# Optimization experiments

Measured on AMD Instinct MI355X. Metric: run time of the kernel, lower is better.

The kernel has to match this reference:

```python
import jax, jax.numpy as jnp
import numpy as np

N = 200000
E = 5000000


def _gcn_norm(edge_index, num_nodes):
    # add self-loops and compute symmetric normalization (PyG GCNConv default)
    loop = jnp.arange(num_nodes, dtype=edge_index.dtype)
    src = jnp.concatenate([edge_index[0], loop])
    dst = jnp.concatenate([edge_index[1], loop])
    ones = jnp.ones(dst.shape[0], dtype=jnp.float32)
    deg = jax.ops.segment_sum(ones, dst, num_segments=num_nodes)
    dis = jnp.where(deg > 0, jax.lax.rsqrt(deg), 0.0)
    norm = dis[src] * dis[dst]  # [E+N]
    return src, dst, norm


def _gcn_layer(x, src, dst, norm, W, b, num_nodes):
    xl = x @ W  # [N, out] dense linear (no bias, PyG default)
    msg = xl[src] * norm[:, None]  # gather + scale
    agg = jax.ops.segment_sum(msg, dst, num_segments=num_nodes)  # scatter-add
    return agg + b


def setup_inputs() -> dict:
    key = jax.random.key(0)
    ks = jax.random.split(key, 10)
    x = jax.random.normal(ks[0], (N, 12), dtype=jnp.float32)
    edge_index = jax.random.randint(ks[1], (2, E), 0, N, dtype=jnp.int64)
    def glorot(k, fi, fo):
        s = np.sqrt(6.0 / (fi + fo)).astype(np.float32)
        return jax.random.uniform(k, (fi, fo), jnp.float32, -s, s)
    return {
        "x": x,
        "edge_index": edge_index,
        "W1": glorot(ks[2], 12, 16), "b1": jnp.zeros((16,), jnp.float32),
        "W2": glorot(ks[3], 16, 8), "b2": jnp.zeros((8,), jnp.float32),
        "W3": glorot(ks[4], 8, 16), "b3": jnp.zeros((16,), jnp.float32),
        "W4": glorot(ks[5], 16, 12), "b4": jnp.zeros((12,), jnp.float32),
    }


def reference(x, edge_index, W1, b1, W2, b2, W3, b3, W4, b4):
    num_nodes = x.shape[0]
    src, dst, norm = _gcn_norm(edge_index, num_nodes)
    # Encoder
    h = jax.nn.relu(_gcn_layer(x, src, dst, norm, W1, b1, num_nodes))
    h = _gcn_layer(h, src, dst, norm, W2, b2, num_nodes)
    # Decoder
    h = jax.nn.relu(_gcn_layer(h, src, dst, norm, W3, b3, num_nodes))
    h = jax.nn.sigmoid(_gcn_layer(h, src, dst, norm, W4, b4, num_nodes))
    return h
```

## Files before the change

### kernel.cpp

```cpp
#include <hip/hip_runtime.h>
#include <hip/hip_fp16.h>
#include <math.h>


#define NPB 1024
#define MAX_NB 256
#define CAP 26496
#define BIN_CHUNK 4096
#define BIN_TH 512
#define EPT (BIN_CHUNK / BIN_TH)
#define MAXB CAP

__global__ void init_cur_kernel(int* __restrict__ bucket_cur, int NB) {
    int t = blockIdx.x * blockDim.x + threadIdx.x;
    if (t < NB) bucket_cur[t] = t * CAP;
}

__global__ __launch_bounds__(BIN_TH) void bin_kernel(const int* __restrict__ src,
                                                     const int* __restrict__ dst,
                                                     int* __restrict__ bucket_cur,
                                                     unsigned int* __restrict__ binned,
                                                     int E, int NB) {
    __shared__ int h[MAX_NB];
    __shared__ int scl[MAX_NB + 1];
    __shared__ int base[MAX_NB];
    __shared__ int sscan[256];
    __shared__ unsigned int stage[BIN_CHUNK];
    __shared__ unsigned char bkt8[BIN_CHUNK];
    int cbeg = blockIdx.x * BIN_CHUNK;
    int cend = min(cbeg + BIN_CHUNK, E);
    int chunk_n = cend - cbeg;
    int tid = threadIdx.x;

    for (int t = tid; t < NB; t += BIN_TH) h[t] = 0;
    __syncthreads();
    int myd[EPT];
#pragma unroll
    for (int j = 0; j < EPT; j++) {
        int e = cbeg + tid + j * BIN_TH;
        if (e < cend) {
            myd[j] = dst[e];
            atomicAdd(&h[myd[j] >> 10], 1);
        }
    }
    __syncthreads();
    int v = (tid < NB) ? h[tid] : 0;
    if (tid < 256) sscan[tid] = v;
    __syncthreads();
    for (int off = 1; off < 256; off <<= 1) {
        int t = (tid >= off && tid < 256) ? sscan[tid - off] : 0;
        __syncthreads();
        if (tid < 256) sscan[tid] += t;
        __syncthreads();
    }
    if (tid < NB) {
        scl[tid] = sscan[tid] - v;
        base[tid] = v ? atomicAdd(&bucket_cur[tid], v) : 0;
    }
    if (tid == 0) scl[NB] = chunk_n;
    __syncthreads();
    for (int t = tid; t < NB; t += BIN_TH) h[t] = 0;
    __syncthreads();
#pragma unroll
    for (int j = 0; j < EPT; j++) {
        int e = cbeg + tid + j * BIN_TH;
        if (e < cend) {
            int d = myd[j];
            int bkt = d >> 10;
            int pos = scl[bkt] + atomicAdd(&h[bkt], 1);
            stage[pos] = ((unsigned)src[e] << 10) | (unsigned)(d & 1023);
            bkt8[pos] = (unsigned char)bkt;
        }
    }
    __syncthreads();
    for (int k = tid; k < chunk_n; k += BIN_TH) {
        int bkt = bkt8[k];
        binned[base[bkt] + (k - scl[bkt])] = stage[k];
    }
}

__global__ __launch_bounds__(1024) void csr_bucket_t1_kernel(
    const unsigned int* __restrict__ binned,
    const int* __restrict__ bucket_cur,
    int2* __restrict__ rows, int* __restrict__ mids, float* __restrict__ dis,
    int* __restrict__ col,
    const float* __restrict__ x,
    __half* __restrict__ xls, int N, int halfN) {
    __shared__ int cnt[NPB];
    __shared__ int cnt0[NPB];
    __shared__ int curA[NPB];
    __shared__ int curB[NPB];
    __shared__ int colbuf[MAXB];
    int b = blockIdx.x;
    int nbase = b << 10;
    int nlocal = min(NPB, N - nbase);
    int beg = b * CAP;
    int bsize = bucket_cur[b] - beg;
    int tid = threadIdx.x;

    cnt[tid] = 0;
    cnt0[tid] = 0;
    __syncthreads();
    for (int k = tid; k < bsize; k += 1024) {
        unsigned rec = binned[beg + k];
        int l = rec & 1023u;
        int s = (int)(rec >> 10);
        atomicAdd(&cnt[l], 1);
        if (s < halfN) atomicAdd(&cnt0[l], 1);
    }
    __syncthreads();
    int v = cnt[tid];
    int v0 = cnt0[tid];
    curA[tid] = v;
    __syncthreads();
    for (int off = 1; off < 1024; off <<= 1) {
        int t = (tid >= off) ? curA[tid - off] : 0;
        __syncthreads();
        curA[tid] += t;
        __syncthreads();
    }
    int excl = curA[tid] - v;
    float d = 1.0f / sqrtf((float)(v + 1));
    if (tid < nlocal) {
        rows[nbase + tid] = make_int2(beg + excl, beg + excl + v);
        mids[nbase + tid] = beg + excl + v0;
        dis[nbase + tid] = d;
    }
    __syncthreads();
    curA[tid] = excl;
    curB[tid] = excl + v0;
    __syncthreads();
    if (bsize <= MAXB) {
        for (int k = tid; k < bsize; k += 1024) {
            unsigned rec = binned[beg + k];
            int l = rec & 1023u;
            int s = (int)(rec >> 10);
            int pos = (s < halfN) ? atomicAdd(&curA[l], 1)
                                  : atomicAdd(&curB[l], 1);
            colbuf[pos] = s;
        }
        __syncthreads();
        for (int k = tid; k < bsize; k += 1024) col[beg + k] = colbuf[k];
    } else {
        for (int k = tid; k < bsize; k += 1024) {
            unsigned rec = binned[beg + k];
            int l = rec & 1023u;
            int s = (int)(rec >> 10);
            int pos = (s < halfN) ? atomicAdd(&curA[l], 1)
                                  : atomicAdd(&curB[l], 1);
            col[beg + pos] = s;
        }
    }
    if (tid < nlocal) {
        int i = nbase + tid;
        float h[12];
#pragma unroll
        for (int k = 0; k < 12; k++) h[k] = x[(size_t)i * 12 + k];
        __half2* x2 = (__half2*)xls;
#pragma unroll
        for (int k = 0; k < 6; k++) {
            x2[(size_t)i * 8 + k] =
                __floats2half2_rn(h[2 * k] * d, h[2 * k + 1] * d);
        }
    }
}

template <int P, int S>
__device__ __forceinline__ void acc_node(const __half2* __restrict__ x2, int c,
                                         float2 (&acc)[P]) {
    __half2 t[P];
#pragma unroll
    for (int k = 0; k < P; k++) t[k] = x2[(size_t)c * S + k];
#pragma unroll
    for (int k = 0; k < P; k++) {
        float2 v = __half22float2(t[k]);
        acc[k].x += v.x;
        acc[k].y += v.y;
    }
}

template <int P, int S>
__device__ __forceinline__ void acc_quad(const __half2* __restrict__ x2, int4 c,
                                         float2 (&acc)[P]) {
    __half2 t[4][P];
#pragma unroll
    for (int k = 0; k < P; k++) t[0][k] = x2[(size_t)c.x * S + k];
#pragma unroll
    for (int k = 0; k < P; k++) t[1][k] = x2[(size_t)c.y * S + k];
#pragma unroll
    for (int k = 0; k < P; k++) t[2][k] = x2[(size_t)c.z * S + k];
#pragma unroll
    for (int k = 0; k < P; k++) t[3][k] = x2[(size_t)c.w * S + k];
#pragma unroll
    for (int k = 0; k < P; k++) {
        float2 a0 = __half22float2(t[0][k]), a1 = __half22float2(t[1][k]);
        float2 a2 = __half22float2(t[2][k]), a3 = __half22float2(t[3][k]);
        acc[k].x += (a0.x + a1.x) + (a2.x + a3.x);
        acc[k].y += (a0.y + a1.y) + (a2.y + a3.y);
    }
}

template <int C, int S>
__device__ __forceinline__ void gather_acc_rng(
    int i, int p, int beg, int end, bool self,
    const int* __restrict__ col, const __half2* __restrict__ x2,
    float2 (&acc)[C / 2]) {
    constexpr int P = C / 2;
    constexpr int UN = (P >= 6) ? 2 : 3;
#pragma unroll
    for (int k = 0; k < P; k++) {
        if (self && p == 0) acc[k] = __half22float2(x2[(size_t)i * S + k]);
        else acc[k] = make_float2(0.0f, 0.0f);
    }
    int nedge = end - beg;
    int pre = (4 - (beg & 3)) & 3;
    if (pre > nedge) pre = nedge;
    for (int j = p; j < pre; j += 2) acc_node<P, S>(x2, col[beg + j], acc);
    int abeg = beg + pre;
    int nq = (end - abeg) >> 2;
    int q = p;
    for (; q + 2 * (UN - 1) < nq; q += 2 * UN) {
        int4 cs[UN];
#pragma unroll
        for (int u = 0; u < UN; u++)
            cs[u] = *reinterpret_cast<const int4*>(col + abeg + 4 * (q + 2 * u));
#pragma unroll
        for (int u = 0; u < UN; u++) acc_quad<P, S>(x2, cs[u], acc);
    }
    for (; q < nq; q += 2) {
        int4 ca = *reinterpret_cast<const int4*>(col + abeg + 4 * q);
        acc_quad<P, S>(x2, ca, acc);
    }
    int tbeg = abeg + 4 * nq;
    for (int j = tbeg + p; j < end; j += 2) acc_node<P, S>(x2, col[j], acc);
#pragma unroll
    for (int k = 0; k < P; k++) {
        acc[k].x += __shfl_xor(acc[k].x, 1);
        acc[k].y += __shfl_xor(acc[k].y, 1);
    }
}

__global__ __launch_bounds__(256) void gather12h_kernel(
    const int2* __restrict__ rows, const int* __restrict__ mids,
    const int* __restrict__ col, const __half* __restrict__ xin,
    float* __restrict__ part0, float* __restrict__ part1, int N, int halfN) {
    int grp = blockIdx.x >> 3;
    int sub = blockIdx.x & 7;
    int chunk = sub >> 2;
    int range = (grp << 2) + (sub & 3);
    int t2 = range * 256 + (int)threadIdx.x;
    int i = t2 >> 1;
    int p = t2 & 1;
    if (i >= N) return;
    int2 r = rows[i];
    int m = mids[i];
    int beg = chunk ? m : r.x;
    int end = chunk ? r.y : m;
    bool self = chunk ? (i >= halfN) : (i < halfN);
    float2 acc[6];
    gather_acc_rng<12, 8>(i, p, beg, end, self, col, (const __half2*)xin, acc);
    float* part = chunk ? part1 : part0;
    float2* ap = (float2*)(part + (size_t)i * 12);
#pragma unroll
    for (int k = 0; k < 6; k++) {
        if ((k & 1) == p) ap[k] = acc[k];
    }
}

__global__ __launch_bounds__(256) void transform12_kernel(
    const float* __restrict__ p0, const float* __restrict__ p1,
    const float* __restrict__ b1, const float* __restrict__ W1,
    const float* __restrict__ W2, const float* __restrict__ dis,
    __half* __restrict__ xout, int N) {
    __shared__ float sW1[12 * 16];
    __shared__ float sW2[16 * 8];
    __shared__ float sB[16];
    if (threadIdx.x < 192) sW1[threadIdx.x] = W1[threadIdx.x];
    if (threadIdx.x < 128) sW2[threadIdx.x] = W2[threadIdx.x];
    if (threadIdx.x < 16) sB[threadIdx.x] = b1[threadIdx.x];
    __syncthreads();
    int i = blockIdx.x * blockDim.x + threadIdx.x;
    if (i >= N) return;
    float d = dis[i];
    float A[12];
    const float4* a4 = (const float4*)(p0 + (size_t)i * 12);
    const float4* b4 = (const float4*)(p1 + (size_t)i * 12);
#pragma unroll
    for (int q = 0; q < 3; q++) {
        float4 va = a4[q], vb = b4[q];
        A[4 * q + 0] = (va.x + vb.x) * d;
        A[4 * q + 1] = (va.y + vb.y) * d;
        A[4 * q + 2] = (va.z + vb.z) * d;
        A[4 * q + 3] = (va.w + vb.w) * d;
    }
    float h[16];
#pragma unroll
    for (int f = 0; f < 16; f++) {
        float acc = sB[f];
#pragma unroll
        for (int k = 0; k < 12; k++) acc = fmaf(A[k], sW1[k * 16 + f], acc);
        h[f] = fmaxf(acc, 0.0f);
    }
    __half2* x2 = (__half2*)xout;
#pragma unroll
    for (int k2 = 0; k2 < 4; k2++) {
        float o0 = 0.0f, o1 = 0.0f;
#pragma unroll
        for (int k = 0; k < 16; k++) {
            o0 = fmaf(h[k], sW2[k * 8 + 2 * k2], o0);
            o1 = fmaf(h[k], sW2[k * 8 + 2 * k2 + 1], o1);
        }
        x2[(size_t)i * 4 + k2] = __floats2half2_rn(o0 * d, o1 * d);
    }
}

__global__ __launch_bounds__(256) void gather8_t3_kernel(
    const int2* __restrict__ rows, const int* __restrict__ col,
    const float* __restrict__ dis, const __half* __restrict__ xin,
    const float* __restrict__ b2, __half* __restrict__ xout, int N) {
    int tid = blockIdx.x * blockDim.x + threadIdx.x;
    int i = tid >> 1;
    int p = tid & 1;
    if (i >= N) return;
    int2 r = rows[i];
    float2 acc[4];
    gather_acc_rng<8, 4>(i, p, r.x, r.y, true, col, (const __half2*)xin, acc);
    float d = dis[i];
    __half2* x2o = (__half2*)xout;
#pragma unroll
    for (int k = 0; k < 4; k++) {
        if ((k >> 1) == p) {
            x2o[(size_t)i * 4 + k] =
                __floats2half2_rn((acc[k].x * d + b2[2 * k]) * d,
                                  (acc[k].y * d + b2[2 * k + 1]) * d);
        }
    }
}

__global__ __launch_bounds__(256) void gather8_t4_kernel(
    const int2* __restrict__ rows, const int* __restrict__ col,
    const float* __restrict__ dis, const __half* __restrict__ xin,
    const float* __restrict__ b3, const float* __restrict__ W3,
    const float* __restrict__ W4, __half* __restrict__ xout, int N) {
    __shared__ float sW3[8 * 16];
    __shared__ float sW4[16 * 12];
    __shared__ float sB[16];
    if (threadIdx.x < 128) sW3[threadIdx.x] = W3[threadIdx.x];
    if (threadIdx.x < 192) sW4[threadIdx.x] = W4[threadIdx.x];
    if (threadIdx.x < 16) sB[threadIdx.x] = b3[threadIdx.x];
    __syncthreads();
    int tid = blockIdx.x * blockDim.x + threadIdx.x;
    int i = tid >> 1;
    int p = tid & 1;
    if (i >= N) return;
    int2 r = rows[i];
    float2 acc[4];
    gather_acc_rng<8, 4>(i, p, r.x, r.y, true, col, (const __half2*)xin, acc);
    float d = dis[i];
    float A[8];
#pragma unroll
    for (int k = 0; k < 4; k++) {
        A[2 * k] = acc[k].x * d;
        A[2 * k + 1] = acc[k].y * d;
    }
    float h[8];
#pragma unroll
    for (int f = 0; f < 8; f++) {
        float a = sB[p * 8 + f];
#pragma unroll
        for (int k = 0; k < 8; k++) a = fmaf(A[k], sW3[k * 16 + p * 8 + f], a);
        h[f] = fmaxf(a, 0.0f);
    }
    float o[12];
#pragma unroll
    for (int j = 0; j < 12; j++) {
        float a = 0.0f;
#pragma unroll
        for (int f = 0; f < 8; f++) a = fmaf(h[f], sW4[(p * 8 + f) * 12 + j], a);
        o[j] = a;
    }
#pragma unroll
    for (int j = 0; j < 12; j++) o[j] += __shfl_xor(o[j], 1);
    __half2* x2o = (__half2*)xout;
    if (p == 0) {
#pragma unroll
        for (int k = 0; k < 4; k++) {
            x2o[(size_t)i * 8 + k] =
                __floats2half2_rn(o[2 * k] * d, o[2 * k + 1] * d);
        }
    } else {
#pragma unroll
        for (int k = 0; k < 2; k++) {
            x2o[(size_t)i * 8 + 4 + k] =
                __floats2half2_rn(o[8 + 2 * k] * d, o[9 + 2 * k] * d);
        }
    }
}

__global__ __launch_bounds__(256) void combine_sig_kernel(
    const float* __restrict__ p0, const float* __restrict__ p1,
    const float* __restrict__ dis, const float* __restrict__ bias,
    float* __restrict__ out, int N) {
    __shared__ float sB[12];
    if (threadIdx.x < 12) sB[threadIdx.x] = bias[threadIdx.x];
    __syncthreads();
    int i = blockIdx.x * blockDim.x + threadIdx.x;
    if (i >= N) return;
    float d = dis[i];
    const float4* a4 = (const float4*)(p0 + (size_t)i * 12);
    const float4* b4 = (const float4*)(p1 + (size_t)i * 12);
    float4* o4 = (float4*)(out + (size_t)i * 12);
#pragma unroll
    for (int q = 0; q < 3; q++) {
        float4 va = a4[q], vb = b4[q];
        float4 r;
        r.x = 1.0f / (1.0f + expf(-((va.x + vb.x) * d + sB[4 * q + 0])));
        r.y = 1.0f / (1.0f + expf(-((va.y + vb.y) * d + sB[4 * q + 1])));
        r.z = 1.0f / (1.0f + expf(-((va.z + vb.z) * d + sB[4 * q + 2])));
        r.w = 1.0f / (1.0f + expf(-((va.w + vb.w) * d + sB[4 * q + 3])));
        o4[q] = r;
    }
}

static inline size_t align_up(size_t v, size_t a) { return (v + a - 1) & ~(a - 1); }

extern "C" void kernel_launch(void* const* d_in, const int* in_sizes, int n_in,
                              void* d_out, int out_size, void* d_ws, size_t ws_size,
                              hipStream_t stream) {
    const float* x  = (const float*)d_in[0];
    const int*   ei = (const int*)d_in[1];
    const float* W1 = (const float*)d_in[2];
    const float* b1 = (const float*)d_in[3];
    const float* W2 = (const float*)d_in[4];
    const float* b2 = (const float*)d_in[5];
    const float* W3 = (const float*)d_in[6];
    const float* b3 = (const float*)d_in[7];
    const float* W4 = (const float*)d_in[8];
    const float* b4 = (const float*)d_in[9];
    float* out = (float*)d_out;

    const int N = in_sizes[0] / 12;
    const int E = in_sizes[1] / 2;
    const int halfN = N >> 1;
    const int* src = ei;
    const int* dst = ei + E;
    const int NB = (N + NPB - 1) / NPB;

    char* ws = (char*)d_ws;
    size_t off = 0;
    int* bucket_cur = (int*)(ws + off);   off = align_up(off + (size_t)NB * 4, 256);
    int2* rows = (int2*)(ws + off);       off = align_up(off + (size_t)N * 8, 256);
    int* mids = (int*)(ws + off);         off = align_up(off + (size_t)N * 4, 256);
    float* dis = (float*)(ws + off);      off = align_up(off + (size_t)N * 4, 256);
    unsigned int* binned = (unsigned int*)(ws + off);
    off = align_up(off + ((size_t)NB * CAP + 4096) * 4, 256);
    int* col = (int*)(ws + off);          off = align_up(off + ((size_t)NB * CAP + 4096) * 4, 256);
    __half* xls = (__half*)(ws + off);    off = align_up(off + (size_t)N * 16 * 2, 256);
    __half* xls2 = (__half*)(ws + off);   off = align_up(off + (size_t)N * 16 * 2, 256);
    (void)ws_size; (void)n_in; (void)out_size;

    float* part0 = (float*)binned;
    float* part1 = part0 + (size_t)N * 12;

    const int B = 256;
    auto blocks = [&](long long n) { return (int)((n + B - 1) / B); };
    int nb2 = blocks(2LL * N);
    nb2 = (nb2 + 3) & ~3;
    const int G2 = nb2 * 2;

    init_cur_kernel<<<1, 256, 0, stream>>>(bucket_cur, NB);
    bin_kernel<<<(E + BIN_CHUNK - 1) / BIN_CHUNK, BIN_TH, 0, stream>>>(src, dst, bucket_cur, binned, E, NB);
    csr_bucket_t1_kernel<<<NB, 1024, 0, stream>>>(binned, bucket_cur, rows, mids, dis,
                                                  col, x, xls, N, halfN);

    gather12h_kernel<<<G2, B, 0, stream>>>(rows, mids, col, xls, part0, part1, N, halfN);

    transform12_kernel<<<blocks(N), B, 0, stream>>>(part0, part1, b1, W1, W2, dis, xls2, N);

    gather8_t3_kernel<<<blocks(2LL * N), B, 0, stream>>>(rows, col, dis, xls2, b2, xls, N);

    gather8_t4_kernel<<<blocks(2LL * N), B, 0, stream>>>(rows, col, dis, xls, b3, W3, W4,
                                                         xls2, N);

    gather12h_kernel<<<G2, B, 0, stream>>>(rows, mids, col, xls2, part0, part1, N, halfN);

    combine_sig_kernel<<<blocks(N), B, 0, stream>>>(part0, part1, dis, b4, out, N);
}
```

Measured before the change: 360.4 us.

## Split 12-wide gathers into four source-range chunks for cache locality

The CSR build now sorts each row's neighbors into four source-node quarter ranges instead of halves and records the three split points per node. The 12-feature gather kernels can run one pass per quarter, so each pass touches a smaller slice of the fp16 feature table and should hit cache more often. Partial sums go to four buffers that the transform and sigmoid kernels add together. The costs are more blocks, extra partial-buffer traffic, an integer divide per edge, and a fallback to two chunks when the workspace is too small.

New measurement: 365.6 us. Within noise of the previous version (+1.4%).

```diff
diff --git a/kernel.cpp b/kernel.cpp
--- a/kernel.cpp
+++ b/kernel.cpp
@@ -82,14 +82,12 @@
 __global__ __launch_bounds__(1024) void csr_bucket_t1_kernel(
     const unsigned int* __restrict__ binned,
     const int* __restrict__ bucket_cur,
-    int2* __restrict__ rows, int* __restrict__ mids, float* __restrict__ dis,
+    int2* __restrict__ rows, int4* __restrict__ qmids, float* __restrict__ dis,
     int* __restrict__ col,
     const float* __restrict__ x,
-    __half* __restrict__ xls, int N, int halfN) {
-    __shared__ int cnt[NPB];
-    __shared__ int cnt0[NPB];
-    __shared__ int curA[NPB];
-    __shared__ int curB[NPB];
+    __half* __restrict__ xls, int N, int qN) {
+    __shared__ int cnt4[4 * NPB];
+    __shared__ int sc[NPB];
     __shared__ int colbuf[MAXB];
     int b = blockIdx.x;
     int nbase = b << 10;
@@ -98,45 +96,51 @@
     int bsize = bucket_cur[b] - beg;
     int tid = threadIdx.x;
 
-    cnt[tid] = 0;
-    cnt0[tid] = 0;
+    for (int t = tid; t < 4 * NPB; t += 1024) cnt4[t] = 0;
     __syncthreads();
     for (int k = tid; k < bsize; k += 1024) {
         unsigned rec = binned[beg + k];
         int l = rec & 1023u;
         int s = (int)(rec >> 10);
-        atomicAdd(&cnt[l], 1);
-        if (s < halfN) atomicAdd(&cnt0[l], 1);
-    }
-    __syncthreads();
-    int v = cnt[tid];
-    int v0 = cnt0[tid];
-    curA[tid] = v;
+        int q = s / qN;
+        atomicAdd(&cnt4[q * NPB + l], 1);
+    }
+    __syncthreads();
+    int c0 = cnt4[tid];
+    int c1 = cnt4[NPB + tid];
+    int c2 = cnt4[2 * NPB + tid];
+    int c3 = cnt4[3 * NPB + tid];
+    int v = c0 + c1 + c2 + c3;
+    sc[tid] = v;
     __syncthreads();
     for (int off = 1; off < 1024; off <<= 1) {
-        int t = (tid >= off) ? curA[tid - off] : 0;
+        int t = (tid >= off) ? sc[tid - off] : 0;
         __syncthreads();
-        curA[tid] += t;
+        sc[tid] += t;
         __syncthreads();
     }
-    int excl = curA[tid] - v;
+    int excl = sc[tid] - v;
     float d = 1.0f / sqrtf((float)(v + 1));
     if (tid < nlocal) {
         rows[nbase + tid] = make_int2(beg + excl, beg + excl + v);
-        mids[nbase + tid] = beg + excl + v0;
+        qmids[nbase + tid] = make_int4(beg + excl + c0,
+                                       beg + excl + c0 + c1,
+                                       beg + excl + c0 + c1 + c2, 0);
         dis[nbase + tid] = d;
     }
     __syncthreads();
-    curA[tid] = excl;
-    curB[tid] = excl + v0;
+    cnt4[tid] = excl;
+    cnt4[NPB + tid] = excl + c0;
+    cnt4[2 * NPB + tid] = excl + c0 + c1;
+    cnt4[3 * NPB + tid] = excl + c0 + c1 + c2;
     __syncthreads();
     if (bsize <= MAXB) {
         for (int k = tid; k < bsize; k += 1024) {
             unsigned rec = binned[beg + k];
             int l = rec & 1023u;
             int s = (int)(rec >> 10);
-            int pos = (s < halfN) ? atomicAdd(&curA[l], 1)
-                                  : atomicAdd(&curB[l], 1);
+            int q = s / qN;
+            int pos = atomicAdd(&cnt4[q * NPB + l], 1);
             colbuf[pos] = s;
         }
         __syncthreads();
@@ -146,8 +150,8 @@
             unsigned rec = binned[beg + k];
             int l = rec & 1023u;
             int s = (int)(rec >> 10);
-            int pos = (s < halfN) ? atomicAdd(&curA[l], 1)
-                                  : atomicAdd(&curB[l], 1);
+            int q = s / qN;
+            int pos = atomicAdd(&cnt4[q * NPB + l], 1);
             col[beg + pos] = s;
         }
     }
@@ -240,26 +244,42 @@
     }
 }
 
-__global__ __launch_bounds__(256) void gather12h_kernel(
-    const int2* __restrict__ rows, const int* __restrict__ mids,
+template <int NC>
+__global__ __launch_bounds__(256) void gather12p_kernel(
+    const int2* __restrict__ rows, const int4* __restrict__ qmids,
     const int* __restrict__ col, const __half* __restrict__ xin,
-    float* __restrict__ part0, float* __restrict__ part1, int N, int halfN) {
+    float* __restrict__ part0, float* __restrict__ part1,
+    float* __restrict__ part2, float* __restrict__ part3, int N, int qN) {
     int grp = blockIdx.x >> 3;
     int sub = blockIdx.x & 7;
-    int chunk = sub >> 2;
-    int range = (grp << 2) + (sub & 3);
+    int chunk, range;
+    if (NC == 4) {
+        chunk = sub >> 1;
+        range = (grp << 1) + (sub & 1);
+    } else {
+        chunk = sub >> 2;
+        range = (grp << 2) + (sub & 3);
+    }
     int t2 = range * 256 + (int)threadIdx.x;
     int i = t2 >> 1;
     int p = t2 & 1;
     if (i >= N) return;
     int2 r = rows[i];
-    int m = mids[i];
-    int beg = chunk ? m : r.x;
-    int end = chunk ? r.y : m;
-    bool self = chunk ? (i >= halfN) : (i < halfN);
+    int4 qm = qmids[i];
+    int beg, end;
+    if (NC == 4) {
+        beg = (chunk == 0) ? r.x : (chunk == 1) ? qm.x : (chunk == 2) ? qm.y : qm.z;
+        end = (chunk == 0) ? qm.x : (chunk == 1) ? qm.y : (chunk == 2) ? qm.z : r.y;
+    } else {
+        beg = chunk ? qm.y : r.x;
+        end = chunk ? r.y : qm.y;
+    }
+    int qi = i / qN;
+    bool self = (NC == 4) ? (qi == chunk) : ((qi >> 1) == chunk);
     float2 acc[6];
     gather_acc_rng<12, 8>(i, p, beg, end, self, col, (const __half2*)xin, acc);
-    float* part = chunk ? part1 : part0;
+    float* part = (chunk == 0) ? part0 : (chunk == 1) ? part1
+                 : (chunk == 2) ? part2 : part3;
     float2* ap = (float2*)(part + (size_t)i * 12);
 #pragma unroll
     for (int k = 0; k < 6; k++) {
@@ -267,8 +287,10 @@
     }
 }
 
+template <int NP>
 __global__ __launch_bounds__(256) void transform12_kernel(
     const float* __restrict__ p0, const float* __restrict__ p1,
+    const float* __restrict__ p2, const float* __restrict__ p3,
     const float* __restrict__ b1, const float* __restrict__ W1,
     const float* __restrict__ W2, const float* __restrict__ dis,
     __half* __restrict__ xout, int N) {
@@ -283,15 +305,21 @@
     if (i >= N) return;
     float d = dis[i];
     float A[12];
-    const float4* a4 = (const float4*)(p0 + (size_t)i * 12);
-    const float4* b4 = (const float4*)(p1 + (size_t)i * 12);
 #pragma unroll
     for (int q = 0; q < 3; q++) {
-        float4 va = a4[q], vb = b4[q];
-        A[4 * q + 0] = (va.x + vb.x) * d;
-        A[4 * q + 1] = (va.y + vb.y) * d;
-        A[4 * q + 2] = (va.z + vb.z) * d;
-        A[4 * q + 3] = (va.w + vb.w) * d;
+        float4 va = ((const float4*)(p0 + (size_t)i * 12))[q];
+        float4 vb = ((const float4*)(p1 + (size_t)i * 12))[q];
+        float sx = va.x + vb.x, sy = va.y + vb.y, sz = va.z + vb.z, sw = va.w + vb.w;
+        if (NP == 4) {
+            float4 vc = ((const float4*)(p2 + (size_t)i * 12))[q];
+            float4 vd = ((const float4*)(p3 + (size_t)i * 12))[q];
+            sx += vc.x + vd.x; sy += vc.y + vd.y;
+            sz += vc.z + vd.z; sw += vc.w + vd.w;
+        }
+        A[4 * q + 0] = sx * d;
+        A[4 * q + 1] = sy * d;
+        A[4 * q + 2] = sz * d;
+        A[4 * q + 3] = sw * d;
     }
     float h[16];
 #pragma unroll
@@ -397,8 +425,10 @@
     }
 }
 
+template <int NP>
 __global__ __launch_bounds__(256) void combine_sig_kernel(
     const float* __restrict__ p0, const float* __restrict__ p1,
+    const float* __restrict__ p2, const float* __restrict__ p3,
     const float* __restrict__ dis, const float* __restrict__ bias,
     float* __restrict__ out, int N) {
     __shared__ float sB[12];
@@ -407,17 +437,23 @@
     int i = blockIdx.x * blockDim.x + threadIdx.x;
     if (i >= N) return;
     float d = dis[i];
-    const float4* a4 = (const float4*)(p0 + (size_t)i * 12);
-    const float4* b4 = (const float4*)(p1 + (size_t)i * 12);
     float4* o4 = (float4*)(out + (size_t)i * 12);
 #pragma unroll
     for (int q = 0; q < 3; q++) {
-        float4 va = a4[q], vb = b4[q];
+        float4 va = ((const float4*)(p0 + (size_t)i * 12))[q];
+        float4 vb = ((const float4*)(p1 + (size_t)i * 12))[q];
+        float sx = va.x + vb.x, sy = va.y + vb.y, sz = va.z + vb.z, sw = va.w + vb.w;
+        if (NP == 4) {
+            float4 vc = ((const float4*)(p2 + (size_t)i * 12))[q];
+            float4 vd = ((const float4*)(p3 + (size_t)i * 12))[q];
+            sx += vc.x + vd.x; sy += vc.y + vd.y;
+            sz += vc.z + vd.z; sw += vc.w + vd.w;
+        }
         float4 r;
-        r.x = 1.0f / (1.0f + expf(-((va.x + vb.x) * d + sB[4 * q + 0])));
-        r.y = 1.0f / (1.0f + expf(-((va.y + vb.y) * d + sB[4 * q + 1])));
-        r.z = 1.0f / (1.0f + expf(-((va.z + vb.z) * d + sB[4 * q + 2])));
-        r.w = 1.0f / (1.0f + expf(-((va.w + vb.w) * d + sB[4 * q + 3])));
+        r.x = 1.0f / (1.0f + expf(-(sx * d + sB[4 * q + 0])));
+        r.y = 1.0f / (1.0f + expf(-(sy * d + sB[4 * q + 1])));
+        r.z = 1.0f / (1.0f + expf(-(sz * d + sB[4 * q + 2])));
+        r.w = 1.0f / (1.0f + expf(-(sw * d + sB[4 * q + 3])));
         o4[q] = r;
     }
 }
@@ -441,7 +477,7 @@
 
     const int N = in_sizes[0] / 12;
     const int E = in_sizes[1] / 2;
-    const int halfN = N >> 1;
+    const int qN = (N + 3) >> 2;
     const int* src = ei;
     const int* dst = ei + E;
     const int NB = (N + NPB - 1) / NPB;
@@ -450,39 +486,59 @@
     size_t off = 0;
     int* bucket_cur = (int*)(ws + off);   off = align_up(off + (size_t)NB * 4, 256);
     int2* rows = (int2*)(ws + off);       off = align_up(off + (size_t)N * 8, 256);
-    int* mids = (int*)(ws + off);         off = align_up(off + (size_t)N * 4, 256);
+    int4* qmids = (int4*)(ws + off);      off = align_up(off + (size_t)N * 16, 256);
     float* dis = (float*)(ws + off);      off = align_up(off + (size_t)N * 4, 256);
     unsigned int* binned = (unsigned int*)(ws + off);
     off = align_up(off + ((size_t)NB * CAP + 4096) * 4, 256);
     int* col = (int*)(ws + off);          off = align_up(off + ((size_t)NB * CAP + 4096) * 4, 256);
     __half* xls = (__half*)(ws + off);    off = align_up(off + (size_t)N * 16 * 2, 256);
     __half* xls2 = (__half*)(ws + off);   off = align_up(off + (size_t)N * 16 * 2, 256);
-    (void)ws_size; (void)n_in; (void)out_size;
+    size_t off23 = off;
+    float* part2 = (float*)(ws + off23);
+    size_t off_end = align_up(off23 + (size_t)N * 24 * 4, 256);
+    const bool use4 = (off_end <= ws_size);
+    float* part3 = part2 + (size_t)N * 12;
+    (void)n_in; (void)out_size;
 
     float* part0 = (float*)binned;
     float* part1 = part0 + (size_t)N * 12;
 
     const int B = 256;
     auto blocks = [&](long long n) { return (int)((n + B - 1) / B); };
-    int nb2 = blocks(2LL * N);
-    nb2 = (nb2 + 3) & ~3;
-    const int G2 = nb2 * 2;
+    int R = blocks(2LL * N);
+    R = (R + 3) & ~3;
 
     init_cur_kernel<<<1, 256, 0, stream>>>(bucket_cur, NB);
     bin_kernel<<<(E + BIN_CHUNK - 1) / BIN_CHUNK, BIN_TH, 0, stream>>>(src, dst, bucket_cur, binned, E, NB);
-    csr_bucket_t1_kernel<<<NB, 1024, 0, stream>>>(binned, bucket_cur, rows, mids, dis,
-                                                  col, x, xls, N, halfN);
-
-    gather12h_kernel<<<G2, B, 0, stream>>>(rows, mids, col, xls, part0, part1, N, halfN);
-
-    transform12_kernel<<<blocks(N), B, 0, stream>>>(part0, part1, b1, W1, W2, dis, xls2, N);
+    csr_bucket_t1_kernel<<<NB, 1024, 0, stream>>>(binned, bucket_cur, rows, qmids, dis,
+                                                  col, x, xls, N, qN);
+
+    if (use4) {
+        gather12p_kernel<4><<<R * 4, B, 0, stream>>>(rows, qmids, col, xls,
+                                                     part0, part1, part2, part3, N, qN);
+        transform12_kernel<4><<<blocks(N), B, 0, stream>>>(part0, part1, part2, part3,
+                                                           b1, W1, W2, dis, xls2, N);
+    } else {
+        gather12p_kernel<2><<<R * 2, B, 0, stream>>>(rows, qmids, col, xls,
+                                                     part0, part1, part0, part1, N, qN);
+        transform12_kernel<2><<<blocks(N), B, 0, stream>>>(part0, part1, part0, part1,
+                                                           b1, W1, W2, dis, xls2, N);
+    }
 
     gather8_t3_kernel<<<blocks(2LL * N), B, 0, stream>>>(rows, col, dis, xls2, b2, xls, N);
 
     gather8_t4_kernel<<<blocks(2LL * N), B, 0, stream>>>(rows, col, dis, xls, b3, W3, W4,
                                                          xls2, N);
 
-    gather12h_kernel<<<G2, B, 0, stream>>>(rows, mids, col, xls2, part0, part1, N, halfN);
-
-    combine_sig_kernel<<<blocks(N), B, 0, stream>>>(part0, part1, dis, b4, out, N);
-}
+    if (use4) {
+        gather12p_kernel<4><<<R * 4, B, 0, stream>>>(rows, qmids, col, xls2,
+                                                     part0, part1, part2, part3, N, qN);
+        combine_sig_kernel<4><<<blocks(N), B, 0, stream>>>(part0, part1, part2, part3,
+                                                           dis, b4, out, N);
+    } else {
+        gather12p_kernel<2><<<R * 2, B, 0, stream>>>(rows, qmids, col, xls2,
+                                                     part0, part1, part0, part1, N, qN);
+        combine_sig_kernel<2><<<blocks(N), B, 0, stream>>>(part0, part1, part0, part1,
+                                                           dis, b4, out, N);
+    }
+}
```
